# Kernel tuning notes

Hardware: AMD Instinct MI355X
Metric: run time of the kernel (lower is better)

The kernel has to match this reference:

```python
import jax, jax.numpy as jnp
import numpy as np

EMBED_DIM = 1024
NUM_HEAD = 16
HEAD_DIM = EMBED_DIM // NUM_HEAD
SCALE = HEAD_DIM ** -0.5


def setup_inputs() -> dict:
    key = jax.random.key(0)
    ks = jax.random.split(key, 8)
    B, N, K, D = 2, 2048, 2048, EMBED_DIM
    s = D ** -0.5
    return {
        "x": jax.random.normal(ks[0], (B, N, D), jnp.float32),
        "ctx": jax.random.normal(ks[1], (B, K, D), jnp.float32),
        "Wq": jax.random.normal(ks[2], (D, D), jnp.float32) * s,
        "bq": jnp.zeros((D,), jnp.float32),
        "Wkv": jax.random.normal(ks[3], (D, 2 * D), jnp.float32) * s,
        "bkv": jnp.zeros((2 * D,), jnp.float32),
        "Wproj": jax.random.normal(ks[4], (D, D), jnp.float32) * s,
        "bproj": jnp.zeros((D,), jnp.float32),
    }


def reference(x, ctx, Wq, bq, Wkv, bkv, Wproj, bproj):
    B, N, D = x.shape
    K = ctx.shape[1]
    H, hd = NUM_HEAD, HEAD_DIM
    # Q projection -> [B, H, N, hd]
    q = (x @ Wq + bq).reshape(B, N, H, hd).transpose(0, 2, 1, 3)
    # KV projection -> k, v each [B, H, K, hd]
    kv = (ctx @ Wkv + bkv).reshape(B, K, 2, H, hd).transpose(2, 0, 3, 1, 4)
    k, v = kv[0], kv[1]
    # scaled dot-product attention with materialized scores [B, H, N, K]
    attn = jnp.einsum("bhnd,bhkd->bhnk", q * SCALE, k)
    attn = jax.nn.softmax(attn, axis=-1)
    out = jnp.einsum("bhnk,bhkd->bhnd", attn, v)
    out = out.transpose(0, 2, 1, 3).reshape(B, N, D)
    return out @ Wproj + bproj
```

## Files before the change

### kernel.cpp

```cpp
#include <hip/hip_runtime.h>
#include <hip/hip_bf16.h>

typedef __attribute__((ext_vector_type(8))) short bf16x8;
typedef __attribute__((ext_vector_type(4))) float f32x4;
typedef unsigned short u16;
typedef unsigned int u32;

#define NUM_HEAD 16
#define HEAD_DIM 64
#define SEQ_N 2048
#define SEQ_K 2048
#define EMB 1024
#define MROWS 4096
static constexpr float ATTN_SCALE = 0.125f;

__device__ __forceinline__ u16 f2bf(float f) {
  __hip_bfloat16 h = __float2bfloat16(f);
  return *reinterpret_cast<u16*>(&h);
}

__device__ __forceinline__ void async16(const u16* g, u16* l) {
  __builtin_amdgcn_global_load_lds(
      (const __attribute__((address_space(1))) unsigned int*)g,
      (__attribute__((address_space(3))) unsigned int*)l, 16, 0, 0);
}

__global__ __launch_bounds__(256) void cvt2(const float* __restrict__ x,
                                            const float* __restrict__ ctx,
                                            u16* __restrict__ xb, u16* __restrict__ cb) {
  const int n4 = MROWS * EMB / 4;
  int gid = blockIdx.x * 256 + threadIdx.x;
  const float4* s; ushort4* d; int i;
  if (gid < n4) { s = (const float4*)x;   d = (ushort4*)xb; i = gid; }
  else          { s = (const float4*)ctx; d = (ushort4*)cb; i = gid - n4; }
  float4 v = s[i];
  ushort4 o;
  o.x = f2bf(v.x); o.y = f2bf(v.y); o.z = f2bf(v.z); o.w = f2bf(v.w);
  d[i] = o;
}

__global__ __launch_bounds__(256) void transpose_cvt4(
    const float* __restrict__ Wq, const float* __restrict__ Wkv,
    const float* __restrict__ Wproj,
    u16* __restrict__ Wqt, u16* __restrict__ Wkvt, u16* __restrict__ Wpt) {
  __shared__ float tile[32][33];
  const int z = blockIdx.z;
  const float* W; u16* Wt; int srcN, colbase;
  if (z == 0)      { W = Wq;    Wt = Wqt;                          srcN = 1024; colbase = 0; }
  else if (z == 1) { W = Wkv;   Wt = Wkvt;                         srcN = 2048; colbase = 0; }
  else if (z == 2) { W = Wkv;   Wt = Wkvt + (size_t)1024 * 1024;   srcN = 2048; colbase = 1024; }
  else             { W = Wproj; Wt = Wpt;                          srcN = 1024; colbase = 0; }
  int n0 = blockIdx.x * 32, k0 = blockIdx.y * 32;
  int tx = threadIdx.x & 31, ty = threadIdx.x >> 5;
  #pragma unroll
  for (int i = ty; i < 32; i += 8)
    tile[i][tx] = W[(size_t)(k0 + i) * srcN + colbase + n0 + tx];
  __syncthreads();
  #pragma unroll
  for (int i = ty; i < 32; i += 8)
    Wt[(size_t)(n0 + i) * 1024 + k0 + tx] = f2bf(tile[tx][i]);
}

__global__ __launch_bounds__(256) void gemm_qkv(
    const u16* __restrict__ xb, const u16* __restrict__ cb,
    const u16* __restrict__ Wqt, const u16* __restrict__ Wkvt,
    const float* __restrict__ bq, const float* __restrict__ bkv,
    u16* __restrict__ Qb, u16* __restrict__ Kb, u16* __restrict__ Vtb)
{
  __shared__ alignas(16) u16 smem[128 * 64 * 2];
  u16* As = smem;
  u16* Bs = smem + 128 * 64;
  const int tid = threadIdx.x;
  const bool isQ = (blockIdx.x < 8);
  const int n0 = (isQ ? blockIdx.x : blockIdx.x - 8) * 128;
  const int m0 = blockIdx.y * 128;
  const u16* A     = isQ ? xb : cb;
  const u16* Wt    = isQ ? Wqt : Wkvt;
  const float* bias = isQ ? bq : bkv;
  const int wave = tid >> 6, lane = tid & 63;
  const int wm = (wave >> 1) * 64, wn = (wave & 1) * 64;
  const int l15 = lane & 15, quad = lane >> 4;

  f32x4 acc[4][4];
  #pragma unroll
  for (int i = 0; i < 4; i++)
    #pragma unroll
    for (int j = 0; j < 4; j++)
      #pragma unroll
      for (int r = 0; r < 4; r++) acc[i][j][r] = 0.0f;

  const int srow = tid >> 3;
  const int scol = (tid & 7) * 8;
  const u16* ag = A + (size_t)(m0 + srow) * EMB + scol;
  const u16* bg = Wt + (size_t)(n0 + srow) * EMB + scol;
  const int ldsoff = tid * 8;

  for (int kt = 0; kt < EMB; kt += 64) {
    #pragma unroll
    for (int s = 0; s < 4; s++) {
      async16(ag + (size_t)(s * 32) * EMB + kt, &As[ldsoff + s * 2048]);
      async16(bg + (size_t)(s * 32) * EMB + kt, &Bs[ldsoff + s * 2048]);
    }
    __syncthreads();
    #pragma unroll
    for (int ks = 0; ks < 2; ks++) {
      bf16x8 af[4], bfr[4];
      #pragma unroll
      for (int i = 0; i < 4; i++) {
        af[i]  = *(const bf16x8*)&As[(wm + i * 16 + l15) * 64 + ks * 32 + quad * 8];
        bfr[i] = *(const bf16x8*)&Bs[(wn + i * 16 + l15) * 64 + ks * 32 + quad * 8];
      }
      #pragma unroll
      for (int i = 0; i < 4; i++)
        #pragma unroll
        for (int j = 0; j < 4; j++)
          acc[i][j] = __builtin_amdgcn_mfma_f32_16x16x32_bf16(af[i], bfr[j], acc[i][j], 0, 0, 0);
    }
    __syncthreads();
  }

  if (isQ) {
    #pragma unroll
    for (int i = 0; i < 4; i++) {
      #pragma unroll
      for (int j = 0; j < 4; j++) {
        const int gc = n0 + wn + j * 16 + l15;
        const float bv = bias[gc];
        const int h = gc >> 6, d = gc & 63;
        #pragma unroll
        for (int r = 0; r < 4; r++) {
          const int gm = m0 + wm + i * 16 + quad * 4 + r;
          const int bb = gm >> 11, nn = gm & 2047;
          Qb[((size_t)(bb * NUM_HEAD + h) * SEQ_N + nn) * HEAD_DIM + d] =
              f2bf((acc[i][j][r] + bv) * ATTN_SCALE);
        }
      }
    }
  } else {
    const int s = (n0 + wn) >> 10;
    if (s == 0) {
      #pragma unroll
      for (int i = 0; i < 4; i++) {
        #pragma unroll
        for (int j = 0; j < 4; j++) {
          const int gc = n0 + wn + j * 16 + l15;
          const float bv = bias[gc];
          const int h = gc >> 6, d = gc & 63;
          #pragma unroll
          for (int r = 0; r < 4; r++) {
            const int gm = m0 + wm + i * 16 + quad * 4 + r;
            const int bb = gm >> 11, kk = gm & 2047;
            Kb[((size_t)(bb * NUM_HEAD + h) * SEQ_K + kk) * HEAD_DIM + d] =
                f2bf(acc[i][j][r] + bv);
          }
        }
      }
    } else {
      u16* wbuf = smem + wave * 2560;
      const int gm0 = m0 + wm;
      const int bb = gm0 >> 11;
      const int kk0 = gm0 & 2047;
      const int hh = ((n0 + wn) >> 6) & 15;
      #pragma unroll
      for (int p = 0; p < 2; p++) {
        #pragma unroll
        for (int jj = 0; jj < 2; jj++) {
          const int j = p * 2 + jj;
          const int gc = n0 + wn + j * 16 + l15;
          const float bv = bias[gc];
          #pragma unroll
          for (int i = 0; i < 4; i++) {
            #pragma unroll
            for (int r = 0; r < 4; r++) {
              wbuf[(jj * 16 + l15) * 72 + i * 16 + quad * 4 + r] = f2bf(acc[i][j][r] + bv);
            }
          }
        }
        __syncthreads();
        u32* dst = (u32*)(Vtb + ((size_t)(bb * NUM_HEAD + hh) * HEAD_DIM + p * 32) * SEQ_K + kk0);
        #pragma unroll
        for (int it = 0; it < 16; it++) {
          const int dd = it * 2 + (lane >> 5);
          const int kp = (lane & 31) * 2;
          u32 v = *(const u32*)&wbuf[dd * 72 + kp];
          dst[((size_t)dd * SEQ_K + kp) >> 1] = v;
        }
        __syncthreads();
      }
    }
  }
}

__global__ __launch_bounds__(256) void gemm_proj(
    const u16* __restrict__ A, const u16* __restrict__ Wt,
    const float* __restrict__ bias, float* __restrict__ outF)
{
  __shared__ alignas(16) u16 smem[(64 + 128) * 64];
  u16* As = smem;
  u16* Bs = smem + 64 * 64;
  const int tid = threadIdx.x;
  const int n0 = blockIdx.x * 128, m0 = blockIdx.y * 64;
  const int wave = tid >> 6, lane = tid & 63;
  const int wm = (wave >> 1) * 32, wn = (wave & 1) * 64;
  const int l15 = lane & 15, quad = lane >> 4;

  f32x4 acc[2][4];
  #pragma unroll
  for (int i = 0; i < 2; i++)
    #pragma unroll
    for (int j = 0; j < 4; j++)
      #pragma unroll
      for (int r = 0; r < 4; r++) acc[i][j][r] = 0.0f;

  const int srow = tid >> 3;
  const int scol = (tid & 7) * 8;
  const u16* ag = A + (size_t)(m0 + srow) * EMB + scol;
  const u16* bg = Wt + (size_t)(n0 + srow) * EMB + scol;
  const int ldsoff = tid * 8;

  for (int kt = 0; kt < EMB; kt += 64) {
    async16(ag + kt, &As[ldsoff]);
    async16(ag + (size_t)32 * EMB + kt, &As[ldsoff + 2048]);
    #pragma unroll
    for (int s = 0; s < 4; s++)
      async16(bg + (size_t)(s * 32) * EMB + kt, &Bs[ldsoff + s * 2048]);
    __syncthreads();
    #pragma unroll
    for (int ks = 0; ks < 2; ks++) {
      bf16x8 af[2], bfr[4];
      #pragma unroll
      for (int i = 0; i < 2; i++)
        af[i]  = *(const bf16x8*)&As[(wm + i * 16 + l15) * 64 + ks * 32 + quad * 8];
      #pragma unroll
      for (int j = 0; j < 4; j++)
        bfr[j] = *(const bf16x8*)&Bs[(wn + j * 16 + l15) * 64 + ks * 32 + quad * 8];
      #pragma unroll
      for (int i = 0; i < 2; i++)
        #pragma unroll
        for (int j = 0; j < 4; j++)
          acc[i][j] = __builtin_amdgcn_mfma_f32_16x16x32_bf16(af[i], bfr[j], acc[i][j], 0, 0, 0);
    }
    __syncthreads();
  }

  #pragma unroll
  for (int i = 0; i < 2; i++) {
    #pragma unroll
    for (int j = 0; j < 4; j++) {
      const int gc = n0 + wn + j * 16 + l15;
      const float bv = bias[gc];
      #pragma unroll
      for (int r = 0; r < 4; r++) {
        const int gm = m0 + wm + i * 16 + quad * 4 + r;
        outF[(size_t)gm * EMB + gc] = acc[i][j][r] + bv;
      }
    }
  }
}

__global__ __launch_bounds__(256) void attn_kernel(
    const u16* __restrict__ Qb, const u16* __restrict__ Kb,
    const u16* __restrict__ Vtb, u16* __restrict__ Ob)
{
  __shared__ alignas(16) u16 Ks[64 * 72];
  __shared__ alignas(16) u16 Vs[64 * 72];
  __shared__ alignas(16) u16 Ps[4 * 32 * 72];
  const int tid = threadIdx.x;
  const int bh = blockIdx.x;
  const int m0 = blockIdx.y * 128;
  const int wave = tid >> 6, lane = tid & 63;
  const int l15 = lane & 15, quad = lane >> 4;
  const int rowb = m0 + wave * 32;

  bf16x8 bq[2][2];
  #pragma unroll
  for (int rs = 0; rs < 2; rs++) {
    const u16* qp = Qb + ((size_t)bh * SEQ_N + rowb + rs * 16 + l15) * HEAD_DIM + quad * 8;
    bq[rs][0] = *(const bf16x8*)(qp);
    bq[rs][1] = *(const bf16x8*)(qp + 32);
  }

  f32x4 o[2][4];
  #pragma unroll
  for (int rs = 0; rs < 2; rs++)
    #pragma unroll
    for (int dt = 0; dt < 4; dt++)
      #pragma unroll
      for (int r = 0; r < 4; r++) o[rs][dt][r] = 0.0f;
  float l_part[2] = {0.f, 0.f};
  u16* pbuf = Ps + wave * 32 * 72;

  const int kr = tid >> 3;
  const int ko = (tid & 7) * 8;
  const u16* kg = Kb + ((size_t)bh * SEQ_K + kr) * HEAD_DIM + ko;
  const u16* vg = Vtb + ((size_t)bh * HEAD_DIM + kr) * SEQ_K + ko;

  uint4 kA = *(const uint4*)(kg);
  uint4 kB = *(const uint4*)(kg + (size_t)32 * HEAD_DIM);
  uint4 vA = *(const uint4*)(vg);
  uint4 vB = *(const uint4*)(vg + (size_t)32 * SEQ_K);

  for (int kt = 0; kt < SEQ_K; kt += 64) {
    *(uint4*)&Ks[kr * 72 + ko]        = kA;
    *(uint4*)&Ks[(kr + 32) * 72 + ko] = kB;
    *(uint4*)&Vs[kr * 72 + ko]        = vA;
    *(uint4*)&Vs[(kr + 32) * 72 + ko] = vB;
    __syncthreads();

    if (kt + 64 < SEQ_K) {
      kA = *(const uint4*)(kg + (size_t)(kt + 64) * HEAD_DIM);
      kB = *(const uint4*)(kg + (size_t)(kt + 96) * HEAD_DIM);
      vA = *(const uint4*)(vg + kt + 64);
      vB = *(const uint4*)(vg + (size_t)32 * SEQ_K + kt + 64);
    }

    #pragma unroll
    for (int kt4 = 0; kt4 < 4; kt4++) {
      const bf16x8 a0 = *(const bf16x8*)&Ks[(kt4 * 16 + l15) * 72 + quad * 8];
      const bf16x8 a1 = *(const bf16x8*)&Ks[(kt4 * 16 + l15) * 72 + 32 + quad * 8];
      #pragma unroll
      for (int rs = 0; rs < 2; rs++) {
        f32x4 z = {0.f, 0.f, 0.f, 0.f};
        z = __builtin_amdgcn_mfma_f32_16x16x32_bf16(a0, bq[rs][0], z, 0, 0, 0);
        z = __builtin_amdgcn_mfma_f32_16x16x32_bf16(a1, bq[rs][1], z, 0, 0, 0);
        ushort4 pk;
        float p0 = __expf(z[0]), p1 = __expf(z[1]);
        float p2 = __expf(z[2]), p3 = __expf(z[3]);
        l_part[rs] += (p0 + p1) + (p2 + p3);
        pk.x = f2bf(p0); pk.y = f2bf(p1); pk.z = f2bf(p2); pk.w = f2bf(p3);
        *(ushort4*)&pbuf[(rs * 16 + l15) * 72 + kt4 * 16 + quad * 4] = pk;
      }
    }

    bf16x8 ap[2][2];
    #pragma unroll
    for (int rs = 0; rs < 2; rs++) {
      ap[rs][0] = *(const bf16x8*)&pbuf[(rs * 16 + l15) * 72 + quad * 8];
      ap[rs][1] = *(const bf16x8*)&pbuf[(rs * 16 + l15) * 72 + 32 + quad * 8];
    }
    #pragma unroll
    for (int dt = 0; dt < 4; dt++) {
      const bf16x8 v0 = *(const bf16x8*)&Vs[(dt * 16 + l15) * 72 + quad * 8];
      const bf16x8 v1 = *(const bf16x8*)&Vs[(dt * 16 + l15) * 72 + 32 + quad * 8];
      #pragma unroll
      for (int rs = 0; rs < 2; rs++) {
        o[rs][dt] = __builtin_amdgcn_mfma_f32_16x16x32_bf16(ap[rs][0], v0, o[rs][dt], 0, 0, 0);
        o[rs][dt] = __builtin_amdgcn_mfma_f32_16x16x32_bf16(ap[rs][1], v1, o[rs][dt], 0, 0, 0);
      }
    }
    __syncthreads();
  }

  float lsum[2];
  #pragma unroll
  for (int rs = 0; rs < 2; rs++) {
    float s = l_part[rs];
    s += __shfl_xor(s, 16, 64);
    s += __shfl_xor(s, 32, 64);
    lsum[rs] = s;
  }

  const int bb = bh >> 4, hh = bh & 15;
  #pragma unroll
  for (int rs = 0; rs < 2; rs++) {
    #pragma unroll
    for (int r = 0; r < 4; r++) {
      const float lv = __shfl(lsum[rs], quad * 4 + r, 64);
      const float inv = 1.0f / lv;
      const int gm = rowb + rs * 16 + quad * 4 + r;
      u16* op = Ob + ((size_t)bb * SEQ_N + gm) * EMB + hh * HEAD_DIM;
      #pragma unroll
      for (int dt = 0; dt < 4; dt++)
        op[dt * 16 + l15] = f2bf(o[rs][dt][r] * inv);
    }
  }
}

extern "C" void kernel_launch(void* const* d_in, const int* in_sizes, int n_in,
                              void* d_out, int out_size, void* d_ws, size_t ws_size,
                              hipStream_t stream)
{
  const float* x     = (const float*)d_in[0];
  const float* ctx   = (const float*)d_in[1];
  const float* Wq    = (const float*)d_in[2];
  const float* bq    = (const float*)d_in[3];
  const float* Wkv   = (const float*)d_in[4];
  const float* bkv   = (const float*)d_in[5];
  const float* Wproj = (const float*)d_in[6];
  const float* bproj = (const float*)d_in[7];
  float* out = (float*)d_out;

  char* ws = (char*)d_ws;
  size_t off = 0;
  auto walloc = [&](size_t bytes) -> void* {
    void* p = ws + off;
    off += (bytes + 255) & ~(size_t)255;
    return p;
  };
  u16* xb   = (u16*)walloc((size_t)MROWS * EMB * 2);
  u16* cb   = (u16*)walloc((size_t)MROWS * EMB * 2);
  u16* Wqt  = (u16*)walloc((size_t)EMB * EMB * 2);
  u16* Wkvt = (u16*)walloc((size_t)2 * EMB * EMB * 2);
  u16* Wpt  = (u16*)walloc((size_t)EMB * EMB * 2);
  u16* Qb   = (u16*)walloc((size_t)MROWS * EMB * 2);
  u16* Kb   = (u16*)walloc((size_t)MROWS * EMB * 2);
  u16* Vtb  = (u16*)walloc((size_t)MROWS * EMB * 2);
  u16* Ob   = (u16*)walloc((size_t)MROWS * EMB * 2);

  cvt2<<<8192, 256, 0, stream>>>(x, ctx, xb, cb);
  transpose_cvt4<<<dim3(32, 32, 4), 256, 0, stream>>>(Wq, Wkv, Wproj, Wqt, Wkvt, Wpt);
  gemm_qkv<<<dim3(24, 32), 256, 0, stream>>>(xb, cb, Wqt, Wkvt, bq, bkv, Qb, Kb, Vtb);
  attn_kernel<<<dim3(32, 16), 256, 0, stream>>>(Qb, Kb, Vtb, Ob);
  gemm_proj<<<dim3(8, 64), 256, 0, stream>>>(Ob, Wpt, bproj, out);
}
```

Before: 229.2 us.

## Split attention key range across waves and reduce partial outputs in LDS

The attention kernel now gives each block 64 query rows and has each of the four waves handle a quarter of the key sequence, loading K and V fragments directly from global memory instead of staging them through shared memory with block-wide barriers. Partial output accumulators and row sums are combined at the end through a sequential LDS reduction across waves. The softmax exponent switches to exp2 with log2(e) folded into the Q scaling, and the launch bounds and grid are adjusted to double the block count. This removes the per-tile __syncthreads, but each wave reads K and V uncached by LDS, uses more registers, and adds a serialized reduction epilogue.

```diff
diff --git a/kernel.cpp b/kernel.cpp
--- a/kernel.cpp
+++ b/kernel.cpp
@@ -12,7 +12,7 @@
 #define SEQ_K 2048
 #define EMB 1024
 #define MROWS 4096
-static constexpr float ATTN_SCALE = 0.125f;
+static constexpr float ATTN_SCALE_LOG2E = 0.125f * 1.44269504f;
 
 __device__ __forceinline__ u16 f2bf(float f) {
   __hip_bfloat16 h = __float2bfloat16(f);
@@ -132,7 +132,7 @@
           const int gm = m0 + wm + i * 16 + quad * 4 + r;
           const int bb = gm >> 11, nn = gm & 2047;
           Qb[((size_t)(bb * NUM_HEAD + h) * SEQ_N + nn) * HEAD_DIM + d] =
-              f2bf((acc[i][j][r] + bv) * ATTN_SCALE);
+              f2bf((acc[i][j][r] + bv) * ATTN_SCALE_LOG2E);
         }
       }
     }
@@ -258,120 +258,139 @@
   }
 }
 
-__global__ __launch_bounds__(256) void attn_kernel(
+__global__ __launch_bounds__(256, 3) void attn_kernel(
     const u16* __restrict__ Qb, const u16* __restrict__ Kb,
     const u16* __restrict__ Vtb, u16* __restrict__ Ob)
 {
-  __shared__ alignas(16) u16 Ks[64 * 72];
-  __shared__ alignas(16) u16 Vs[64 * 72];
-  __shared__ alignas(16) u16 Ps[4 * 32 * 72];
+  __shared__ alignas(16) u16 Ps[4 * 64 * 72];
   const int tid = threadIdx.x;
   const int bh = blockIdx.x;
-  const int m0 = blockIdx.y * 128;
+  const int m0 = blockIdx.y * 64;
   const int wave = tid >> 6, lane = tid & 63;
   const int l15 = lane & 15, quad = lane >> 4;
-  const int rowb = m0 + wave * 32;
-
-  bf16x8 bq[2][2];
-  #pragma unroll
-  for (int rs = 0; rs < 2; rs++) {
-    const u16* qp = Qb + ((size_t)bh * SEQ_N + rowb + rs * 16 + l15) * HEAD_DIM + quad * 8;
+
+  const u16* kbase = Kb + (size_t)bh * SEQ_K * HEAD_DIM;
+  const u16* vbase = Vtb + (size_t)bh * HEAD_DIM * SEQ_K;
+
+  bf16x8 bq[4][2];
+  #pragma unroll
+  for (int rs = 0; rs < 4; rs++) {
+    const u16* qp = Qb + ((size_t)bh * SEQ_N + m0 + rs * 16 + l15) * HEAD_DIM + quad * 8;
     bq[rs][0] = *(const bf16x8*)(qp);
     bq[rs][1] = *(const bf16x8*)(qp + 32);
   }
 
-  f32x4 o[2][4];
-  #pragma unroll
-  for (int rs = 0; rs < 2; rs++)
+  f32x4 o[4][4];
+  #pragma unroll
+  for (int rs = 0; rs < 4; rs++)
     #pragma unroll
     for (int dt = 0; dt < 4; dt++)
       #pragma unroll
       for (int r = 0; r < 4; r++) o[rs][dt][r] = 0.0f;
-  float l_part[2] = {0.f, 0.f};
-  u16* pbuf = Ps + wave * 32 * 72;
-
-  const int kr = tid >> 3;
-  const int ko = (tid & 7) * 8;
-  const u16* kg = Kb + ((size_t)bh * SEQ_K + kr) * HEAD_DIM + ko;
-  const u16* vg = Vtb + ((size_t)bh * HEAD_DIM + kr) * SEQ_K + ko;
-
-  uint4 kA = *(const uint4*)(kg);
-  uint4 kB = *(const uint4*)(kg + (size_t)32 * HEAD_DIM);
-  uint4 vA = *(const uint4*)(vg);
-  uint4 vB = *(const uint4*)(vg + (size_t)32 * SEQ_K);
-
-  for (int kt = 0; kt < SEQ_K; kt += 64) {
-    *(uint4*)&Ks[kr * 72 + ko]        = kA;
-    *(uint4*)&Ks[(kr + 32) * 72 + ko] = kB;
-    *(uint4*)&Vs[kr * 72 + ko]        = vA;
-    *(uint4*)&Vs[(kr + 32) * 72 + ko] = vB;
-    __syncthreads();
-
-    if (kt + 64 < SEQ_K) {
-      kA = *(const uint4*)(kg + (size_t)(kt + 64) * HEAD_DIM);
-      kB = *(const uint4*)(kg + (size_t)(kt + 96) * HEAD_DIM);
-      vA = *(const uint4*)(vg + kt + 64);
-      vB = *(const uint4*)(vg + (size_t)32 * SEQ_K + kt + 64);
-    }
+  float l_part[4] = {0.f, 0.f, 0.f, 0.f};
+  u16* pbuf = Ps + wave * 64 * 72;
+
+  for (int t = 0; t < 8; t++) {
+    const int kt = (wave * 8 + t) * 64;
 
     #pragma unroll
     for (int kt4 = 0; kt4 < 4; kt4++) {
-      const bf16x8 a0 = *(const bf16x8*)&Ks[(kt4 * 16 + l15) * 72 + quad * 8];
-      const bf16x8 a1 = *(const bf16x8*)&Ks[(kt4 * 16 + l15) * 72 + 32 + quad * 8];
-      #pragma unroll
-      for (int rs = 0; rs < 2; rs++) {
+      const u16* kp = kbase + (size_t)(kt + kt4 * 16 + l15) * HEAD_DIM + quad * 8;
+      const bf16x8 a0 = *(const bf16x8*)(kp);
+      const bf16x8 a1 = *(const bf16x8*)(kp + 32);
+      #pragma unroll
+      for (int rs = 0; rs < 4; rs++) {
         f32x4 z = {0.f, 0.f, 0.f, 0.f};
         z = __builtin_amdgcn_mfma_f32_16x16x32_bf16(a0, bq[rs][0], z, 0, 0, 0);
         z = __builtin_amdgcn_mfma_f32_16x16x32_bf16(a1, bq[rs][1], z, 0, 0, 0);
+        float p0 = exp2f(z[0]), p1 = exp2f(z[1]);
+        float p2 = exp2f(z[2]), p3 = exp2f(z[3]);
+        l_part[rs] += (p0 + p1) + (p2 + p3);
         ushort4 pk;
-        float p0 = __expf(z[0]), p1 = __expf(z[1]);
-        float p2 = __expf(z[2]), p3 = __expf(z[3]);
-        l_part[rs] += (p0 + p1) + (p2 + p3);
         pk.x = f2bf(p0); pk.y = f2bf(p1); pk.z = f2bf(p2); pk.w = f2bf(p3);
         *(ushort4*)&pbuf[(rs * 16 + l15) * 72 + kt4 * 16 + quad * 4] = pk;
       }
     }
 
-    bf16x8 ap[2][2];
-    #pragma unroll
-    for (int rs = 0; rs < 2; rs++) {
+    bf16x8 ap[4][2];
+    #pragma unroll
+    for (int rs = 0; rs < 4; rs++) {
       ap[rs][0] = *(const bf16x8*)&pbuf[(rs * 16 + l15) * 72 + quad * 8];
       ap[rs][1] = *(const bf16x8*)&pbuf[(rs * 16 + l15) * 72 + 32 + quad * 8];
     }
     #pragma unroll
     for (int dt = 0; dt < 4; dt++) {
-      const bf16x8 v0 = *(const bf16x8*)&Vs[(dt * 16 + l15) * 72 + quad * 8];
-      const bf16x8 v1 = *(const bf16x8*)&Vs[(dt * 16 + l15) * 72 + 32 + quad * 8];
-      #pragma unroll
-      for (int rs = 0; rs < 2; rs++) {
+      const u16* vp = vbase + (size_t)(dt * 16 + l15) * SEQ_K + kt + quad * 8;
+      const bf16x8 v0 = *(const bf16x8*)(vp);
+      const bf16x8 v1 = *(const bf16x8*)(vp + 32);
+      #pragma unroll
+      for (int rs = 0; rs < 4; rs++) {
         o[rs][dt] = __builtin_amdgcn_mfma_f32_16x16x32_bf16(ap[rs][0], v0, o[rs][dt], 0, 0, 0);
         o[rs][dt] = __builtin_amdgcn_mfma_f32_16x16x32_bf16(ap[rs][1], v1, o[rs][dt], 0, 0, 0);
       }
     }
-    __syncthreads();
-  }
-
-  float lsum[2];
-  #pragma unroll
-  for (int rs = 0; rs < 2; rs++) {
+  }
+
+  float lsum[4];
+  #pragma unroll
+  for (int rs = 0; rs < 4; rs++) {
     float s = l_part[rs];
     s += __shfl_xor(s, 16, 64);
     s += __shfl_xor(s, 32, 64);
     lsum[rs] = s;
   }
 
-  const int bb = bh >> 4, hh = bh & 15;
-  #pragma unroll
-  for (int rs = 0; rs < 2; rs++) {
-    #pragma unroll
-    for (int r = 0; r < 4; r++) {
-      const float lv = __shfl(lsum[rs], quad * 4 + r, 64);
-      const float inv = 1.0f / lv;
-      const int gm = rowb + rs * 16 + quad * 4 + r;
-      u16* op = Ob + ((size_t)bb * SEQ_N + gm) * EMB + hh * HEAD_DIM;
+  __syncthreads();
+  float* rbuf = (float*)Ps;
+  float* rl   = rbuf + 64 * 68;
+
+  if (wave == 3) {
+    #pragma unroll
+    for (int rs = 0; rs < 4; rs++) {
       #pragma unroll
       for (int dt = 0; dt < 4; dt++)
-        op[dt * 16 + l15] = f2bf(o[rs][dt][r] * inv);
+        #pragma unroll
+        for (int r = 0; r < 4; r++)
+          rbuf[(rs * 16 + quad * 4 + r) * 68 + dt * 16 + l15] = o[rs][dt][r];
+      if (quad == 0) rl[rs * 16 + l15] = lsum[rs];
+    }
+  }
+  __syncthreads();
+  #pragma unroll
+  for (int w = 2; w >= 1; w--) {
+    if (wave == w) {
+      #pragma unroll
+      for (int rs = 0; rs < 4; rs++) {
+        #pragma unroll
+        for (int dt = 0; dt < 4; dt++)
+          #pragma unroll
+          for (int r = 0; r < 4; r++) {
+            const int idx = (rs * 16 + quad * 4 + r) * 68 + dt * 16 + l15;
+            rbuf[idx] += o[rs][dt][r];
+          }
+        if (quad == 0) rl[rs * 16 + l15] += lsum[rs];
+      }
+    }
+    __syncthreads();
+  }
+
+  if (wave == 0) {
+    const int bb = bh >> 4, hh = bh & 15;
+    #pragma unroll
+    for (int rs = 0; rs < 4; rs++) {
+      #pragma unroll
+      for (int r = 0; r < 4; r++) {
+        const int row = quad * 4 + r;
+        const float lv = rl[rs * 16 + row] + __shfl(lsum[rs], row, 64);
+        const float inv = 1.0f / lv;
+        const int gm = m0 + rs * 16 + row;
+        u16* op = Ob + ((size_t)bb * SEQ_N + gm) * EMB + hh * HEAD_DIM;
+        #pragma unroll
+        for (int dt = 0; dt < 4; dt++) {
+          const float tot = o[rs][dt][r] + rbuf[(rs * 16 + row) * 68 + dt * 16 + l15];
+          op[dt * 16 + l15] = f2bf(tot * inv);
+        }
+      }
     }
   }
 }
@@ -410,6 +429,6 @@
   cvt2<<<8192, 256, 0, stream>>>(x, ctx, xb, cb);
   transpose_cvt4<<<dim3(32, 32, 4), 256, 0, stream>>>(Wq, Wkv, Wproj, Wqt, Wkvt, Wpt);
   gemm_qkv<<<dim3(24, 32), 256, 0, stream>>>(xb, cb, Wqt, Wkvt, bq, bkv, Qb, Kb, Vtb);
-  attn_kernel<<<dim3(32, 16), 256, 0, stream>>>(Qb, Kb, Vtb, Ob);
+  attn_kernel<<<dim3(32, 32), 256, 0, stream>>>(Qb, Kb, Vtb, Ob);
   gemm_proj<<<dim3(8, 64), 256, 0, stream>>>(Ob, Wpt, bproj, out);
 }
```

Result: slower. 304.4 us (+32.8%).

## Retile QKV GEMM to 64x256 blocks and fold log2e into Q scale

Applied to the files above, without the earlier changes.

The QKV projection GEMM moves from 128x128 to 64x256 block tiles. Each wave now computes 32x128, the V-transpose epilogue is reworked per head with packed LDS writes, and the grid becomes 12x64 with launch bounds requesting 3 blocks per CU. Separately, log2(e) is folded into the Q scaling so the attention kernel can use exp2f instead of __expf. The retiling changes data reuse and occupancy, with more B-tile loads per block, and the exp2 change trims a multiply from the softmax inner loop.

```diff
diff --git a/kernel.cpp b/kernel.cpp
--- a/kernel.cpp
+++ b/kernel.cpp
@@ -12,7 +12,7 @@
 #define SEQ_K 2048
 #define EMB 1024
 #define MROWS 4096
-static constexpr float ATTN_SCALE = 0.125f;
+static constexpr float ATTN_SCALE_LOG2E = 0.125f * 1.44269504f;
 
 __device__ __forceinline__ u16 f2bf(float f) {
   __hip_bfloat16 h = __float2bfloat16(f);
@@ -61,31 +61,31 @@
     Wt[(size_t)(n0 + i) * 1024 + k0 + tx] = f2bf(tile[tx][i]);
 }
 
-__global__ __launch_bounds__(256) void gemm_qkv(
+__global__ __launch_bounds__(256, 3) void gemm_qkv(
     const u16* __restrict__ xb, const u16* __restrict__ cb,
     const u16* __restrict__ Wqt, const u16* __restrict__ Wkvt,
     const float* __restrict__ bq, const float* __restrict__ bkv,
     u16* __restrict__ Qb, u16* __restrict__ Kb, u16* __restrict__ Vtb)
 {
-  __shared__ alignas(16) u16 smem[128 * 64 * 2];
+  __shared__ alignas(16) u16 smem[(64 + 256) * 64];
   u16* As = smem;
-  u16* Bs = smem + 128 * 64;
+  u16* Bs = smem + 64 * 64;
   const int tid = threadIdx.x;
-  const bool isQ = (blockIdx.x < 8);
-  const int n0 = (isQ ? blockIdx.x : blockIdx.x - 8) * 128;
-  const int m0 = blockIdx.y * 128;
-  const u16* A     = isQ ? xb : cb;
-  const u16* Wt    = isQ ? Wqt : Wkvt;
+  const bool isQ = (blockIdx.x < 4);
+  const int n0 = (isQ ? blockIdx.x : blockIdx.x - 4) * 256;
+  const int m0 = blockIdx.y * 64;
+  const u16* A      = isQ ? xb : cb;
+  const u16* Wt     = isQ ? Wqt : Wkvt;
   const float* bias = isQ ? bq : bkv;
   const int wave = tid >> 6, lane = tid & 63;
-  const int wm = (wave >> 1) * 64, wn = (wave & 1) * 64;
+  const int wm = (wave >> 1) * 32, wn = (wave & 1) * 128;
   const int l15 = lane & 15, quad = lane >> 4;
 
-  f32x4 acc[4][4];
-  #pragma unroll
-  for (int i = 0; i < 4; i++)
-    #pragma unroll
-    for (int j = 0; j < 4; j++)
+  f32x4 acc[2][8];
+  #pragma unroll
+  for (int i = 0; i < 2; i++)
+    #pragma unroll
+    for (int j = 0; j < 8; j++)
       #pragma unroll
       for (int r = 0; r < 4; r++) acc[i][j][r] = 0.0f;
 
@@ -97,23 +97,25 @@
 
   for (int kt = 0; kt < EMB; kt += 64) {
     #pragma unroll
-    for (int s = 0; s < 4; s++) {
+    for (int s = 0; s < 2; s++)
       async16(ag + (size_t)(s * 32) * EMB + kt, &As[ldsoff + s * 2048]);
+    #pragma unroll
+    for (int s = 0; s < 8; s++)
       async16(bg + (size_t)(s * 32) * EMB + kt, &Bs[ldsoff + s * 2048]);
-    }
     __syncthreads();
     #pragma unroll
     for (int ks = 0; ks < 2; ks++) {
-      bf16x8 af[4], bfr[4];
-      #pragma unroll
-      for (int i = 0; i < 4; i++) {
+      bf16x8 af[2], bfr[8];
+      #pragma unroll
+      for (int i = 0; i < 2; i++)
         af[i]  = *(const bf16x8*)&As[(wm + i * 16 + l15) * 64 + ks * 32 + quad * 8];
-        bfr[i] = *(const bf16x8*)&Bs[(wn + i * 16 + l15) * 64 + ks * 32 + quad * 8];
-      }
-      #pragma unroll
-      for (int i = 0; i < 4; i++)
+      #pragma unroll
+      for (int j = 0; j < 8; j++)
+        bfr[j] = *(const bf16x8*)&Bs[(wn + j * 16 + l15) * 64 + ks * 32 + quad * 8];
+      #pragma unroll
+      for (int i = 0; i < 2; i++)
         #pragma unroll
-        for (int j = 0; j < 4; j++)
+        for (int j = 0; j < 8; j++)
           acc[i][j] = __builtin_amdgcn_mfma_f32_16x16x32_bf16(af[i], bfr[j], acc[i][j], 0, 0, 0);
     }
     __syncthreads();
@@ -121,9 +123,9 @@
 
   if (isQ) {
     #pragma unroll
-    for (int i = 0; i < 4; i++) {
-      #pragma unroll
-      for (int j = 0; j < 4; j++) {
+    for (int i = 0; i < 2; i++) {
+      #pragma unroll
+      for (int j = 0; j < 8; j++) {
         const int gc = n0 + wn + j * 16 + l15;
         const float bv = bias[gc];
         const int h = gc >> 6, d = gc & 63;
@@ -132,17 +134,17 @@
           const int gm = m0 + wm + i * 16 + quad * 4 + r;
           const int bb = gm >> 11, nn = gm & 2047;
           Qb[((size_t)(bb * NUM_HEAD + h) * SEQ_N + nn) * HEAD_DIM + d] =
-              f2bf((acc[i][j][r] + bv) * ATTN_SCALE);
+              f2bf((acc[i][j][r] + bv) * ATTN_SCALE_LOG2E);
         }
       }
     }
   } else {
-    const int s = (n0 + wn) >> 10;
+    const int s = n0 >> 10;
     if (s == 0) {
       #pragma unroll
-      for (int i = 0; i < 4; i++) {
+      for (int i = 0; i < 2; i++) {
         #pragma unroll
-        for (int j = 0; j < 4; j++) {
+        for (int j = 0; j < 8; j++) {
           const int gc = n0 + wn + j * 16 + l15;
           const float bv = bias[gc];
           const int h = gc >> 6, d = gc & 63;
@@ -156,36 +158,42 @@
         }
       }
     } else {
-      u16* wbuf = smem + wave * 2560;
+      u16* wbuf = smem + wave * 1280;
       const int gm0 = m0 + wm;
       const int bb = gm0 >> 11;
       const int kk0 = gm0 & 2047;
-      const int hh = ((n0 + wn) >> 6) & 15;
-      #pragma unroll
-      for (int p = 0; p < 2; p++) {
+      const int hbase = ((n0 + wn) >> 6) & 15;
+      #pragma unroll
+      for (int hh2 = 0; hh2 < 2; hh2++) {
         #pragma unroll
-        for (int jj = 0; jj < 2; jj++) {
-          const int j = p * 2 + jj;
-          const int gc = n0 + wn + j * 16 + l15;
-          const float bv = bias[gc];
+        for (int p = 0; p < 2; p++) {
           #pragma unroll
-          for (int i = 0; i < 4; i++) {
+          for (int jj = 0; jj < 2; jj++) {
+            const int j = hh2 * 4 + p * 2 + jj;
+            const int gc = n0 + wn + j * 16 + l15;
+            const float bv = bias[gc];
             #pragma unroll
-            for (int r = 0; r < 4; r++) {
-              wbuf[(jj * 16 + l15) * 72 + i * 16 + quad * 4 + r] = f2bf(acc[i][j][r] + bv);
+            for (int i = 0; i < 2; i++) {
+              ushort4 pk;
+              pk.x = f2bf(acc[i][j][0] + bv);
+              pk.y = f2bf(acc[i][j][1] + bv);
+              pk.z = f2bf(acc[i][j][2] + bv);
+              pk.w = f2bf(acc[i][j][3] + bv);
+              *(ushort4*)&wbuf[(jj * 16 + l15) * 40 + i * 16 + quad * 4] = pk;
             }
           }
+          __syncthreads();
+          u32* dstu = (u32*)(Vtb +
+              ((size_t)(bb * NUM_HEAD + hbase + hh2) * HEAD_DIM + p * 32) * SEQ_K + kk0);
+          #pragma unroll
+          for (int it = 0; it < 8; it++) {
+            const int dd = it * 4 + quad;
+            const int kp = l15 * 2;
+            u32 v = *(const u32*)&wbuf[dd * 40 + kp];
+            dstu[(size_t)dd * (SEQ_K / 2) + (kp >> 1)] = v;
+          }
+          __syncthreads();
         }
-        __syncthreads();
-        u32* dst = (u32*)(Vtb + ((size_t)(bb * NUM_HEAD + hh) * HEAD_DIM + p * 32) * SEQ_K + kk0);
-        #pragma unroll
-        for (int it = 0; it < 16; it++) {
-          const int dd = it * 2 + (lane >> 5);
-          const int kp = (lane & 31) * 2;
-          u32 v = *(const u32*)&wbuf[dd * 72 + kp];
-          dst[((size_t)dd * SEQ_K + kp) >> 1] = v;
-        }
-        __syncthreads();
       }
     }
   }
@@ -324,8 +332,8 @@
         z = __builtin_amdgcn_mfma_f32_16x16x32_bf16(a0, bq[rs][0], z, 0, 0, 0);
         z = __builtin_amdgcn_mfma_f32_16x16x32_bf16(a1, bq[rs][1], z, 0, 0, 0);
         ushort4 pk;
-        float p0 = __expf(z[0]), p1 = __expf(z[1]);
-        float p2 = __expf(z[2]), p3 = __expf(z[3]);
+        float p0 = exp2f(z[0]), p1 = exp2f(z[1]);
+        float p2 = exp2f(z[2]), p3 = exp2f(z[3]);
         l_part[rs] += (p0 + p1) + (p2 + p3);
         pk.x = f2bf(p0); pk.y = f2bf(p1); pk.z = f2bf(p2); pk.w = f2bf(p3);
         *(ushort4*)&pbuf[(rs * 16 + l15) * 72 + kt4 * 16 + quad * 4] = pk;
@@ -409,7 +417,7 @@
 
   cvt2<<<8192, 256, 0, stream>>>(x, ctx, xb, cb);
   transpose_cvt4<<<dim3(32, 32, 4), 256, 0, stream>>>(Wq, Wkv, Wproj, Wqt, Wkvt, Wpt);
-  gemm_qkv<<<dim3(24, 32), 256, 0, stream>>>(xb, cb, Wqt, Wkvt, bq, bkv, Qb, Kb, Vtb);
+  gemm_qkv<<<dim3(12, 64), 256, 0, stream>>>(xb, cb, Wqt, Wkvt, bq, bkv, Qb, Kb, Vtb);
   attn_kernel<<<dim3(32, 16), 256, 0, stream>>>(Qb, Kb, Vtb, Ob);
   gemm_proj<<<dim3(8, 64), 256, 0, stream>>>(Ob, Wpt, bproj, out);
 }
```

Result: no change. 232.7 us (+1.5%).
